# Optimization experiments

Hardware: AMD Instinct MI355X
Metric: run time of the kernel (lower is better)

The kernel has to match this reference:

```python
import jax, jax.numpy as jnp
import numpy as np

N, E, F, H, C = 50000, 800000, 128, 128, 40


def gcn_conv(x, edge_index, W, b):
    """PyG-style GCNConv: add self-loops, symmetric normalization, scatter-add."""
    n = x.shape[0]
    loop = jnp.arange(n, dtype=edge_index.dtype)
    src = jnp.concatenate([edge_index[0], loop])  # [E+N] source nodes
    dst = jnp.concatenate([edge_index[1], loop])  # [E+N] target nodes
    deg = jax.ops.segment_sum(jnp.ones_like(src, dtype=x.dtype), dst, num_segments=n)
    dinv = jnp.where(deg > 0, jax.lax.rsqrt(jnp.maximum(deg, 1e-12)), 0.0)
    norm = dinv[src] * dinv[dst]                  # [E+N]
    h = x @ W                                     # [N, out]
    msg = h[src] * norm[:, None]                  # [E+N, out]
    return jax.ops.segment_sum(msg, dst, num_segments=n) + b


def setup_inputs() -> dict:
    key = jax.random.key(0)
    ks = jax.random.split(key, 8)
    x = jax.random.normal(ks[0], (N, F), dtype=jnp.float32)
    edge_index = jax.random.randint(ks[1], (2, E), 0, N, dtype=jnp.int32)
    s = lambda fan_in: 1.0 / np.sqrt(fan_in)
    W1 = jax.random.normal(ks[2], (F, H), dtype=jnp.float32) * s(F)
    b1 = jax.random.normal(ks[3], (H,), dtype=jnp.float32) * 0.01
    W2 = jax.random.normal(ks[4], (H, C), dtype=jnp.float32) * s(H)
    b2 = jax.random.normal(ks[5], (C,), dtype=jnp.float32) * 0.01
    Wlin = jax.random.normal(ks[6], (C, C), dtype=jnp.float32) * s(C)
    blin = jax.random.normal(ks[7], (C,), dtype=jnp.float32) * 0.01
    return {"x": x, "edge_index": edge_index, "W1": W1, "b1": b1,
            "W2": W2, "b2": b2, "Wlin": Wlin, "blin": blin}


def reference(x, edge_index, W1, b1, W2, b2, Wlin, blin):
    h1 = jax.nn.relu(gcn_conv(x, edge_index, W1, b1))
    h2 = jax.nn.relu(gcn_conv(h1, edge_index, W2, b2))
    out = h2 @ Wlin + blin
    return (h2, out)
```

## Files before the change

### kernel.cpp

```cpp
#include <hip/hip_runtime.h>


constexpr int FDIM = 128;
constexpr int CDIM = 40;
constexpr int NPB  = 64;
constexpr int MAXNB = 1024;
constexpr int CH   = 4096;

typedef _Float16 h8  __attribute__((ext_vector_type(8)));
typedef _Float16 h4  __attribute__((ext_vector_type(4)));
typedef float    f4  __attribute__((ext_vector_type(4)));

static inline size_t AL512(size_t x) { return (x + 511) & ~size_t(511); }

__global__ __launch_bounds__(256) void k_bhist(const int* __restrict__ dst,
        int* __restrict__ bcnt, int E, int nb) {
    __shared__ int h[MAXNB];
    for (int i = threadIdx.x; i < nb; i += 256) h[i] = 0;
    __syncthreads();
    for (int i = blockIdx.x * 256 + threadIdx.x; i < E; i += gridDim.x * 256)
        atomicAdd(&h[dst[i] >> 6], 1);
    __syncthreads();
    for (int i = threadIdx.x; i < nb; i += 256) {
        int c = h[i];
        if (c) atomicAdd(&bcnt[i], c);
    }
}

__global__ __launch_bounds__(1024) void k_bscan(const int* __restrict__ bcnt,
        int* __restrict__ bbase, int* __restrict__ bcur, int nb, int E) {
    __shared__ int tmp[1024];
    int t = threadIdx.x;
    int v = (t < nb) ? bcnt[t] : 0;
    tmp[t] = v;
    __syncthreads();
    for (int o = 1; o < 1024; o <<= 1) {
        int u = (t >= o) ? tmp[t - o] : 0;
        __syncthreads();
        tmp[t] += u;
        __syncthreads();
    }
    if (t < nb) { int b = tmp[t] - v; bbase[t] = b; bcur[t] = b; }
    if (t == 0) bbase[nb] = E;
}

__global__ __launch_bounds__(256) void k_partition(const int* __restrict__ src,
        const int* __restrict__ dst, int* __restrict__ bcur,
        unsigned* __restrict__ eb, int E, int nb) {
    __shared__ int hcnt[MAXNB];
    __shared__ int gb[MAXNB];
    int e0 = blockIdx.x * CH;
    int cnt = min(CH, E - e0);
    for (int i = threadIdx.x; i < nb; i += 256) hcnt[i] = 0;
    __syncthreads();
    for (int i = threadIdx.x; i < cnt; i += 256)
        atomicAdd(&hcnt[dst[e0 + i] >> 6], 1);
    __syncthreads();
    for (int i = threadIdx.x; i < nb; i += 256) {
        int c = hcnt[i];
        if (c) gb[i] = atomicAdd(&bcur[i], c);
        hcnt[i] = 0;
    }
    __syncthreads();
    for (int i = threadIdx.x; i < cnt; i += 256) {
        int d = dst[e0 + i], b = d >> 6;
        int p = atomicAdd(&hcnt[b], 1);
        eb[gb[b] + p] = ((unsigned)src[e0 + i] << 6) | (unsigned)(d & 63);
    }
}

__global__ __launch_bounds__(256) void k_bucket_csr(const unsigned* __restrict__ eb,
        const int* __restrict__ bbase, int* __restrict__ offs,
        float* __restrict__ dinv, int* __restrict__ ss, int n) {
    __shared__ int cnt[NPB];
    __shared__ int cur[NPB];
    int b = blockIdx.x;
    int beg = bbase[b], end = bbase[b + 1];
    if (threadIdx.x < NPB) cnt[threadIdx.x] = 0;
    __syncthreads();
    for (int i = beg + threadIdx.x; i < end; i += 256)
        atomicAdd(&cnt[eb[i] & 63], 1);
    __syncthreads();
    if (threadIdx.x < NPB) {
        int v = cnt[threadIdx.x];
        int s = v;
#pragma unroll
        for (int o = 1; o < NPB; o <<= 1) {
            int u = __shfl_up(s, o, 64);
            if (threadIdx.x >= (unsigned)o) s += u;
        }
        int e0 = beg + s - v;
        cur[threadIdx.x] = e0;
        int node = b * NPB + threadIdx.x;
        if (node < n) {
            offs[node] = e0;
            dinv[node] = rsqrtf((float)v + 1.0f);
        }
    }
    __syncthreads();
    for (int i = beg + threadIdx.x; i < end; i += 256) {
        unsigned p = eb[i];
        int pos = atomicAdd(&cur[p & 63], 1);
        ss[pos] = (int)(p >> 6);
    }
}

__global__ __launch_bounds__(256) void k_prep(const float* __restrict__ W1,
        const float* __restrict__ W2, _Float16* __restrict__ W1t,
        _Float16* __restrict__ W2t) {
    int i = blockIdx.x * 256 + threadIdx.x;
    if (i < 128 * 128) {
        int c = i >> 7, k = i & 127;
        W1t[c * 128 + k] = (_Float16)W1[k * 128 + c];
    }
    int j = i - 128 * 128;
    if (j >= 0 && j < 64 * 128) {
        int c = j >> 7, k = j & 127;
        W2t[c * 128 + k] = (c < CDIM) ? (_Float16)W2[k * CDIM + c] : (_Float16)0.f;
    }
}

__global__ __launch_bounds__(256) void k_gemm1(const float* __restrict__ X,
        const _Float16* __restrict__ W1t, const float* __restrict__ dinv,
        _Float16* __restrict__ Hp, int n) {
    __shared__ _Float16 xh[64][136];
    __shared__ _Float16 wt[128][136];
    int t = threadIdx.x;
    int r0 = blockIdx.x * 64;
    for (int i = t; i < 64 * 32; i += 256) {
        int r = i >> 5, c4 = (i & 31) * 4;
        int gr = r0 + r;
        float4 v = make_float4(0.f, 0.f, 0.f, 0.f);
        if (gr < n) v = *(const float4*)&X[(size_t)gr * 128 + c4];
        h4 hv; hv[0] = (_Float16)v.x; hv[1] = (_Float16)v.y;
               hv[2] = (_Float16)v.z; hv[3] = (_Float16)v.w;
        *(h4*)&xh[r][c4] = hv;
    }
    for (int i = t; i < 128 * 16; i += 256) {
        int r = i >> 4, c8 = (i & 15) * 8;
        *(uint4*)&wt[r][c8] = *(const uint4*)&W1t[r * 128 + c8];
    }
    __syncthreads();
    int wid = t >> 6, lane = t & 63;
    int fr = lane & 15, fg = lane >> 4;
    f4 acc[8];
#pragma unroll
    for (int ct = 0; ct < 8; ++ct) acc[ct] = (f4){0.f, 0.f, 0.f, 0.f};
#pragma unroll
    for (int ks = 0; ks < 4; ++ks) {
        h8 a = *(const h8*)&xh[wid * 16 + fr][ks * 32 + fg * 8];
#pragma unroll
        for (int ct = 0; ct < 8; ++ct) {
            h8 b = *(const h8*)&wt[ct * 16 + fr][ks * 32 + fg * 8];
            acc[ct] = __builtin_amdgcn_mfma_f32_16x16x32_f16(a, b, acc[ct], 0, 0, 0);
        }
    }
    int rbase = r0 + wid * 16 + fg * 4;
    float dv[4];
#pragma unroll
    for (int rg = 0; rg < 4; ++rg) dv[rg] = (rbase + rg < n) ? dinv[rbase + rg] : 0.f;
#pragma unroll
    for (int ct = 0; ct < 8; ++ct)
#pragma unroll
        for (int rg = 0; rg < 4; ++rg) {
            int gr = rbase + rg;
            if (gr < n) Hp[(size_t)gr * 128 + ct * 16 + fr] = (_Float16)(acc[ct][rg] * dv[rg]);
        }
}

__global__ __launch_bounds__(256) void k_agg128(const int* __restrict__ ss,
        const int* __restrict__ offs, const _Float16* __restrict__ hp,
        const float* __restrict__ b1, const float* __restrict__ dinv,
        _Float16* __restrict__ h1, int n, int E) {
    int w = (blockIdx.x * 256 + threadIdx.x) >> 6;
    int lane = threadIdx.x & 63;
    if (w >= n) return;
    int beg = offs[w];
    int end = (w == n - 1) ? E : offs[w + 1];
    const h8* hpv = (const h8*)hp;
    int g = lane >> 4, c = lane & 15;
    h8 sv = hpv[(size_t)w * 16 + c];
    float acc[8];
#pragma unroll
    for (int i = 0; i < 8; ++i) acc[i] = (g == 0) ? (float)sv[i] : 0.f;
    int j = beg;
    for (; j + 7 < end; j += 8) {
        int s0 = ss[j + g];
        int s1 = ss[j + 4 + g];
        h8 v0 = hpv[(size_t)s0 * 16 + c];
        h8 v1 = hpv[(size_t)s1 * 16 + c];
#pragma unroll
        for (int i = 0; i < 8; ++i) acc[i] += (float)v0[i] + (float)v1[i];
    }
    for (; j < end; j += 4) {
        int idx = j + g;
        if (idx < end) {
            int s = ss[idx];
            h8 v = hpv[(size_t)s * 16 + c];
#pragma unroll
            for (int i = 0; i < 8; ++i) acc[i] += (float)v[i];
        }
    }
#pragma unroll
    for (int i = 0; i < 8; ++i) {
        acc[i] += __shfl_xor(acc[i], 16);
        acc[i] += __shfl_xor(acc[i], 32);
    }
    if (lane < 16) {
        float dvv = dinv[w];
        const float4 bb0 = *(const float4*)&b1[8 * lane];
        const float4 bb1 = *(const float4*)&b1[8 * lane + 4];
        h8 o;
        o[0] = (_Float16)fmaxf(fmaf(dvv, acc[0], bb0.x), 0.f);
        o[1] = (_Float16)fmaxf(fmaf(dvv, acc[1], bb0.y), 0.f);
        o[2] = (_Float16)fmaxf(fmaf(dvv, acc[2], bb0.z), 0.f);
        o[3] = (_Float16)fmaxf(fmaf(dvv, acc[3], bb0.w), 0.f);
        o[4] = (_Float16)fmaxf(fmaf(dvv, acc[4], bb1.x), 0.f);
        o[5] = (_Float16)fmaxf(fmaf(dvv, acc[5], bb1.y), 0.f);
        o[6] = (_Float16)fmaxf(fmaf(dvv, acc[6], bb1.z), 0.f);
        o[7] = (_Float16)fmaxf(fmaf(dvv, acc[7], bb1.w), 0.f);
        *(h8*)&h1[(size_t)w * 128 + 8 * lane] = o;
    }
}

__global__ __launch_bounds__(256) void k_gemm2(const _Float16* __restrict__ H1,
        const _Float16* __restrict__ W2t, const float* __restrict__ dinv,
        _Float16* __restrict__ Hp2, int n) {
    __shared__ _Float16 xh[64][136];
    __shared__ _Float16 wt[64][136];
    int t = threadIdx.x;
    int r0 = blockIdx.x * 64;
    for (int i = t; i < 64 * 16; i += 256) {
        int r = i >> 4, c8 = (i & 15) * 8;
        int gr = r0 + r;
        uint4 v = make_uint4(0u, 0u, 0u, 0u);
        if (gr < n) v = *(const uint4*)&H1[(size_t)gr * 128 + c8];
        *(uint4*)&xh[r][c8] = v;
    }
    for (int i = t; i < 64 * 16; i += 256) {
        int r = i >> 4, c8 = (i & 15) * 8;
        *(uint4*)&wt[r][c8] = *(const uint4*)&W2t[r * 128 + c8];
    }
    __syncthreads();
    int wid = t >> 6, lane = t & 63;
    int fr = lane & 15, fg = lane >> 4;
    f4 acc[4];
#pragma unroll
    for (int ct = 0; ct < 4; ++ct) acc[ct] = (f4){0.f, 0.f, 0.f, 0.f};
#pragma unroll
    for (int ks = 0; ks < 4; ++ks) {
        h8 a = *(const h8*)&xh[wid * 16 + fr][ks * 32 + fg * 8];
#pragma unroll
        for (int ct = 0; ct < 4; ++ct) {
            h8 b = *(const h8*)&wt[ct * 16 + fr][ks * 32 + fg * 8];
            acc[ct] = __builtin_amdgcn_mfma_f32_16x16x32_f16(a, b, acc[ct], 0, 0, 0);
        }
    }
    int rbase = r0 + wid * 16 + fg * 4;
    float dv[4];
#pragma unroll
    for (int rg = 0; rg < 4; ++rg) dv[rg] = (rbase + rg < n) ? dinv[rbase + rg] : 0.f;
#pragma unroll
    for (int ct = 0; ct < 4; ++ct)
#pragma unroll
        for (int rg = 0; rg < 4; ++rg) {
            int gr = rbase + rg;
            if (gr < n) Hp2[(size_t)gr * 64 + ct * 16 + fr] = (_Float16)(acc[ct][rg] * dv[rg]);
        }
}

__global__ __launch_bounds__(256) void k_agg40(const int* __restrict__ ss,
        const int* __restrict__ offs, const _Float16* __restrict__ hp,
        const float* __restrict__ b2, const float* __restrict__ dinv,
        float* __restrict__ h2out, int n, int E) {
    int w = (blockIdx.x * 256 + threadIdx.x) >> 6;
    int lane = threadIdx.x & 63;
    if (w >= n) return;
    int beg = offs[w];
    int end = (w == n - 1) ? E : offs[w + 1];
    const h8* hpv = (const h8*)hp;
    int g = lane >> 3, c = lane & 7;
    h8 sv = hpv[(size_t)w * 8 + c];
    float acc[8];
#pragma unroll
    for (int i = 0; i < 8; ++i) acc[i] = (g == 0) ? (float)sv[i] : 0.f;
    int j = beg;
    for (; j + 15 < end; j += 16) {
        int s0 = ss[j + g];
        int s1 = ss[j + 8 + g];
        h8 v0 = hpv[(size_t)s0 * 8 + c];
        h8 v1 = hpv[(size_t)s1 * 8 + c];
#pragma unroll
        for (int i = 0; i < 8; ++i) acc[i] += (float)v0[i] + (float)v1[i];
    }
    for (; j < end; j += 8) {
        int idx = j + g;
        if (idx < end) {
            int s = ss[idx];
            h8 v = hpv[(size_t)s * 8 + c];
#pragma unroll
            for (int i = 0; i < 8; ++i) acc[i] += (float)v[i];
        }
    }
#pragma unroll
    for (int i = 0; i < 8; ++i) {
        acc[i] += __shfl_xor(acc[i], 8);
        acc[i] += __shfl_xor(acc[i], 16);
        acc[i] += __shfl_xor(acc[i], 32);
    }
    if (lane < 5) {
        float dvv = dinv[w];
        const float4 bb0 = *(const float4*)&b2[8 * lane];
        const float4 bb1 = *(const float4*)&b2[8 * lane + 4];
        float4 r0, r1;
        r0.x = fmaxf(fmaf(dvv, acc[0], bb0.x), 0.f);
        r0.y = fmaxf(fmaf(dvv, acc[1], bb0.y), 0.f);
        r0.z = fmaxf(fmaf(dvv, acc[2], bb0.z), 0.f);
        r0.w = fmaxf(fmaf(dvv, acc[3], bb0.w), 0.f);
        r1.x = fmaxf(fmaf(dvv, acc[4], bb1.x), 0.f);
        r1.y = fmaxf(fmaf(dvv, acc[5], bb1.y), 0.f);
        r1.z = fmaxf(fmaf(dvv, acc[6], bb1.z), 0.f);
        r1.w = fmaxf(fmaf(dvv, acc[7], bb1.w), 0.f);
        *(float4*)&h2out[(size_t)w * CDIM + 8 * lane] = r0;
        *(float4*)&h2out[(size_t)w * CDIM + 8 * lane + 4] = r1;
    }
}

__global__ __launch_bounds__(256) void k_final(const float* __restrict__ h2,
        const float* __restrict__ Wlin, const float* __restrict__ blin,
        float* __restrict__ lin_out, int n) {
    __shared__ float wl[CDIM * CDIM];
    __shared__ float hs[32 * CDIM];
    int t = threadIdx.x;
    int r0 = blockIdx.x * 32;
    for (int i = t; i < CDIM * CDIM; i += 256) wl[i] = Wlin[i];
    int lim = n * CDIM - r0 * CDIM;
    for (int i = t; i < 32 * CDIM; i += 256)
        hs[i] = (i < lim) ? h2[(size_t)r0 * CDIM + i] : 0.f;
    __syncthreads();
    for (int i = t; i < 32 * CDIM; i += 256) {
        int r = i / CDIM, c = i % CDIM;
        int gr = r0 + r;
        if (gr >= n) continue;
        float acc = blin[c];
#pragma unroll
        for (int k = 0; k < CDIM; ++k) acc = fmaf(hs[r * CDIM + k], wl[k * CDIM + c], acc);
        lin_out[(size_t)gr * CDIM + c] = acc;
    }
}

extern "C" void kernel_launch(void* const* d_in, const int* in_sizes, int n_in,
                              void* d_out, int out_size, void* d_ws, size_t ws_size,
                              hipStream_t stream) {
    const float* x    = (const float*)d_in[0];
    const int*   ei   = (const int*)d_in[1];
    const float* W1   = (const float*)d_in[2];
    const float* b1   = (const float*)d_in[3];
    const float* W2   = (const float*)d_in[4];
    const float* b2   = (const float*)d_in[5];
    const float* Wlin = (const float*)d_in[6];
    const float* blin = (const float*)d_in[7];
    float* out = (float*)d_out;

    const int n = in_sizes[0] / FDIM;
    const int E = in_sizes[1] / 2;
    const int* src = ei;
    const int* dst = ei + E;
    const int nb = (n + NPB - 1) / NPB;

    char* ws = (char*)d_ws;
    size_t off = 0;
    int*       bcnt  = (int*)(ws + off);       off = AL512(off + (size_t)nb * 4);
    int*       bbase = (int*)(ws + off);       off = AL512(off + (size_t)(nb + 1) * 4);
    int*       bcur  = (int*)(ws + off);       off = AL512(off + (size_t)nb * 4);
    unsigned*  eb    = (unsigned*)(ws + off);  off = AL512(off + (size_t)E * 4);
    int*       offs  = (int*)(ws + off);       off = AL512(off + (size_t)n * 4);
    int*       ss    = (int*)(ws + off);       off = AL512(off + (size_t)E * 4);
    float*     dinv  = (float*)(ws + off);     off = AL512(off + (size_t)n * 4);
    _Float16*  W1t   = (_Float16*)(ws + off);  off = AL512(off + (size_t)128 * 128 * 2);
    _Float16*  W2t   = (_Float16*)(ws + off);  off = AL512(off + (size_t)64 * 128 * 2);
    _Float16*  hp1   = (_Float16*)(ws + off);  off = AL512(off + (size_t)n * FDIM * 2);
    _Float16*  h1h   = (_Float16*)(ws + off);  off = AL512(off + (size_t)n * FDIM * 2);
    _Float16*  hp2   = (_Float16*)(ws + off);  off = AL512(off + (size_t)n * 64 * 2);
    (void)ws_size; (void)n_in; (void)out_size;

    float* h2_out  = out;
    float* lin_out = out + (size_t)n * CDIM;

    k_prep<<<(128 * 128 + 64 * 128 + 255) / 256, 256, 0, stream>>>(W1, W2, W1t, W2t);
    hipMemsetAsync(bcnt, 0, (size_t)nb * 4, stream);
    k_bhist<<<256, 256, 0, stream>>>(dst, bcnt, E, nb);
    k_bscan<<<1, 1024, 0, stream>>>(bcnt, bbase, bcur, nb, E);
    k_partition<<<(E + CH - 1) / CH, 256, 0, stream>>>(src, dst, bcur, eb, E, nb);
    k_bucket_csr<<<nb, 256, 0, stream>>>(eb, bbase, offs, dinv, ss, n);

    k_gemm1<<<(n + 63) / 64, 256, 0, stream>>>(x, W1t, dinv, hp1, n);
    k_agg128<<<(n * 64 + 255) / 256, 256, 0, stream>>>(ss, offs, hp1, b1, dinv, h1h, n, E);

    k_gemm2<<<(n + 63) / 64, 256, 0, stream>>>(h1h, W2t, dinv, hp2, n);
    k_agg40<<<(n * 64 + 255) / 256, 256, 0, stream>>>(ss, offs, hp2, b2, dinv, h2_out, n, E);

    k_final<<<(n + 31) / 32, 256, 0, stream>>>(h2_out, Wlin, blin, lin_out, n);
}
```

Before: 150.5 us.

## Fuse final linear layer into agg40, fold memset into prep, deepen gather unroll

The final 40x40 linear layer is computed inside the second aggregation kernel. Each wavefront broadcasts its h2 row through shuffles and each lane produces one output column, which removes the k_final launch and the re-read of h2. The bucket-count memset is folded into k_prep to drop one stream operation. Both aggregation kernels gain a 4-way unrolled gather loop so more independent loads are in flight. The cost is extra global Wlin reads per wavefront (cache-resident) and higher register use.

```diff
diff --git a/kernel.cpp b/kernel.cpp
--- a/kernel.cpp
+++ b/kernel.cpp
@@ -12,6 +12,22 @@
 typedef float    f4  __attribute__((ext_vector_type(4)));
 
 static inline size_t AL512(size_t x) { return (x + 511) & ~size_t(511); }
+
+__global__ __launch_bounds__(256) void k_prep(const float* __restrict__ W1,
+        const float* __restrict__ W2, _Float16* __restrict__ W1t,
+        _Float16* __restrict__ W2t, int* __restrict__ bcnt, int nb) {
+    int i = blockIdx.x * 256 + threadIdx.x;
+    if (i < nb) bcnt[i] = 0;
+    if (i < 128 * 128) {
+        int c = i >> 7, k = i & 127;
+        W1t[c * 128 + k] = (_Float16)W1[k * 128 + c];
+    }
+    int j = i - 128 * 128;
+    if (j >= 0 && j < 64 * 128) {
+        int c = j >> 7, k = j & 127;
+        W2t[c * 128 + k] = (c < CDIM) ? (_Float16)W2[k * CDIM + c] : (_Float16)0.f;
+    }
+}
 
 __global__ __launch_bounds__(256) void k_bhist(const int* __restrict__ dst,
         int* __restrict__ bcnt, int E, int nb) {
@@ -102,21 +118,6 @@
         unsigned p = eb[i];
         int pos = atomicAdd(&cur[p & 63], 1);
         ss[pos] = (int)(p >> 6);
-    }
-}
-
-__global__ __launch_bounds__(256) void k_prep(const float* __restrict__ W1,
-        const float* __restrict__ W2, _Float16* __restrict__ W1t,
-        _Float16* __restrict__ W2t) {
-    int i = blockIdx.x * 256 + threadIdx.x;
-    if (i < 128 * 128) {
-        int c = i >> 7, k = i & 127;
-        W1t[c * 128 + k] = (_Float16)W1[k * 128 + c];
-    }
-    int j = i - 128 * 128;
-    if (j >= 0 && j < 64 * 128) {
-        int c = j >> 7, k = j & 127;
-        W2t[c * 128 + k] = (c < CDIM) ? (_Float16)W2[k * CDIM + c] : (_Float16)0.f;
     }
 }
 
@@ -184,6 +185,19 @@
 #pragma unroll
     for (int i = 0; i < 8; ++i) acc[i] = (g == 0) ? (float)sv[i] : 0.f;
     int j = beg;
+    for (; j + 15 < end; j += 16) {
+        int s0 = ss[j + g];
+        int s1 = ss[j + 4 + g];
+        int s2 = ss[j + 8 + g];
+        int s3 = ss[j + 12 + g];
+        h8 v0 = hpv[(size_t)s0 * 16 + c];
+        h8 v1 = hpv[(size_t)s1 * 16 + c];
+        h8 v2 = hpv[(size_t)s2 * 16 + c];
+        h8 v3 = hpv[(size_t)s3 * 16 + c];
+#pragma unroll
+        for (int i = 0; i < 8; ++i)
+            acc[i] += ((float)v0[i] + (float)v1[i]) + ((float)v2[i] + (float)v3[i]);
+    }
     for (; j + 7 < end; j += 8) {
         int s0 = ss[j + g];
         int s1 = ss[j + 4 + g];
@@ -272,7 +286,8 @@
 __global__ __launch_bounds__(256) void k_agg40(const int* __restrict__ ss,
         const int* __restrict__ offs, const _Float16* __restrict__ hp,
         const float* __restrict__ b2, const float* __restrict__ dinv,
-        float* __restrict__ h2out, int n, int E) {
+        const float* __restrict__ Wlin, const float* __restrict__ blin,
+        float* __restrict__ h2out, float* __restrict__ lin_out, int n, int E) {
     int w = (blockIdx.x * 256 + threadIdx.x) >> 6;
     int lane = threadIdx.x & 63;
     if (w >= n) return;
@@ -285,6 +300,19 @@
 #pragma unroll
     for (int i = 0; i < 8; ++i) acc[i] = (g == 0) ? (float)sv[i] : 0.f;
     int j = beg;
+    for (; j + 31 < end; j += 32) {
+        int s0 = ss[j + g];
+        int s1 = ss[j + 8 + g];
+        int s2 = ss[j + 16 + g];
+        int s3 = ss[j + 24 + g];
+        h8 v0 = hpv[(size_t)s0 * 8 + c];
+        h8 v1 = hpv[(size_t)s1 * 8 + c];
+        h8 v2 = hpv[(size_t)s2 * 8 + c];
+        h8 v3 = hpv[(size_t)s3 * 8 + c];
+#pragma unroll
+        for (int i = 0; i < 8; ++i)
+            acc[i] += ((float)v0[i] + (float)v1[i]) + ((float)v2[i] + (float)v3[i]);
+    }
     for (; j + 15 < end; j += 16) {
         int s0 = ss[j + g];
         int s1 = ss[j + 8 + g];
@@ -308,45 +336,39 @@
         acc[i] += __shfl_xor(acc[i], 16);
         acc[i] += __shfl_xor(acc[i], 32);
     }
+    float dvv = dinv[w];
+    float hv[8];
+    if (c < 5) {
+        const float4 bb0 = *(const float4*)&b2[8 * c];
+        const float4 bb1 = *(const float4*)&b2[8 * c + 4];
+        hv[0] = fmaxf(fmaf(dvv, acc[0], bb0.x), 0.f);
+        hv[1] = fmaxf(fmaf(dvv, acc[1], bb0.y), 0.f);
+        hv[2] = fmaxf(fmaf(dvv, acc[2], bb0.z), 0.f);
+        hv[3] = fmaxf(fmaf(dvv, acc[3], bb0.w), 0.f);
+        hv[4] = fmaxf(fmaf(dvv, acc[4], bb1.x), 0.f);
+        hv[5] = fmaxf(fmaf(dvv, acc[5], bb1.y), 0.f);
+        hv[6] = fmaxf(fmaf(dvv, acc[6], bb1.z), 0.f);
+        hv[7] = fmaxf(fmaf(dvv, acc[7], bb1.w), 0.f);
+    } else {
+#pragma unroll
+        for (int i = 0; i < 8; ++i) hv[i] = 0.f;
+    }
     if (lane < 5) {
-        float dvv = dinv[w];
-        const float4 bb0 = *(const float4*)&b2[8 * lane];
-        const float4 bb1 = *(const float4*)&b2[8 * lane + 4];
-        float4 r0, r1;
-        r0.x = fmaxf(fmaf(dvv, acc[0], bb0.x), 0.f);
-        r0.y = fmaxf(fmaf(dvv, acc[1], bb0.y), 0.f);
-        r0.z = fmaxf(fmaf(dvv, acc[2], bb0.z), 0.f);
-        r0.w = fmaxf(fmaf(dvv, acc[3], bb0.w), 0.f);
-        r1.x = fmaxf(fmaf(dvv, acc[4], bb1.x), 0.f);
-        r1.y = fmaxf(fmaf(dvv, acc[5], bb1.y), 0.f);
-        r1.z = fmaxf(fmaf(dvv, acc[6], bb1.z), 0.f);
-        r1.w = fmaxf(fmaf(dvv, acc[7], bb1.w), 0.f);
-        *(float4*)&h2out[(size_t)w * CDIM + 8 * lane] = r0;
-        *(float4*)&h2out[(size_t)w * CDIM + 8 * lane + 4] = r1;
-    }
-}
-
-__global__ __launch_bounds__(256) void k_final(const float* __restrict__ h2,
-        const float* __restrict__ Wlin, const float* __restrict__ blin,
-        float* __restrict__ lin_out, int n) {
-    __shared__ float wl[CDIM * CDIM];
-    __shared__ float hs[32 * CDIM];
-    int t = threadIdx.x;
-    int r0 = blockIdx.x * 32;
-    for (int i = t; i < CDIM * CDIM; i += 256) wl[i] = Wlin[i];
-    int lim = n * CDIM - r0 * CDIM;
-    for (int i = t; i < 32 * CDIM; i += 256)
-        hs[i] = (i < lim) ? h2[(size_t)r0 * CDIM + i] : 0.f;
-    __syncthreads();
-    for (int i = t; i < 32 * CDIM; i += 256) {
-        int r = i / CDIM, c = i % CDIM;
-        int gr = r0 + r;
-        if (gr >= n) continue;
-        float acc = blin[c];
-#pragma unroll
-        for (int k = 0; k < CDIM; ++k) acc = fmaf(hs[r * CDIM + k], wl[k * CDIM + c], acc);
-        lin_out[(size_t)gr * CDIM + c] = acc;
-    }
+        *(float4*)&h2out[(size_t)w * CDIM + 8 * lane] =
+            make_float4(hv[0], hv[1], hv[2], hv[3]);
+        *(float4*)&h2out[(size_t)w * CDIM + 8 * lane + 4] =
+            make_float4(hv[4], hv[5], hv[6], hv[7]);
+    }
+    float o = (lane < CDIM) ? blin[lane] : 0.f;
+#pragma unroll
+    for (int kc = 0; kc < 5; ++kc) {
+#pragma unroll
+        for (int i = 0; i < 8; ++i) {
+            float hk = __shfl(hv[i], kc);
+            if (lane < CDIM) o = fmaf(hk, Wlin[(8 * kc + i) * CDIM + lane], o);
+        }
+    }
+    if (lane < CDIM) lin_out[(size_t)w * CDIM + lane] = o;
 }
 
 extern "C" void kernel_launch(void* const* d_in, const int* in_sizes, int n_in,
@@ -387,8 +409,7 @@
     float* h2_out  = out;
     float* lin_out = out + (size_t)n * CDIM;
 
-    k_prep<<<(128 * 128 + 64 * 128 + 255) / 256, 256, 0, stream>>>(W1, W2, W1t, W2t);
-    hipMemsetAsync(bcnt, 0, (size_t)nb * 4, stream);
+    k_prep<<<(128 * 128 + 64 * 128 + 255) / 256, 256, 0, stream>>>(W1, W2, W1t, W2t, bcnt, nb);
     k_bhist<<<256, 256, 0, stream>>>(dst, bcnt, E, nb);
     k_bscan<<<1, 1024, 0, stream>>>(bcnt, bbase, bcur, nb, E);
     k_partition<<<(E + CH - 1) / CH, 256, 0, stream>>>(src, dst, bcur, eb, E, nb);
@@ -398,7 +419,6 @@
     k_agg128<<<(n * 64 + 255) / 256, 256, 0, stream>>>(ss, offs, hp1, b1, dinv, h1h, n, E);
 
     k_gemm2<<<(n + 63) / 64, 256, 0, stream>>>(h1h, W2t, dinv, hp2, n);
-    k_agg40<<<(n * 64 + 255) / 256, 256, 0, stream>>>(ss, offs, hp2, b2, dinv, h2_out, n, E);
-
-    k_final<<<(n + 31) / 32, 256, 0, stream>>>(h2_out, Wlin, blin, lin_out, n);
-}
+    k_agg40<<<(n * 64 + 255) / 256, 256, 0, stream>>>(ss, offs, hp2, b2, dinv,
+                                                      Wlin, blin, h2_out, lin_out, n, E);
+}
```

Result: slower. 172.1 us (+14.4%).

## Split gathered features into 32-column slabs and narrow neighbor indices to 16-bit

Applied to the files above, without the earlier changes.

Intermediate feature matrices are stored as separate 32-column planes, and aggregation blocks are ordered by plane so that each gather pass works on a smaller table that is more likely to stay cache-resident. Layer 2 is split into a 32-column plane and an 8-column plane, which drops the zero padding to 64 columns. Neighbor indices are stored as 16-bit values, halving index traffic, and the bucket-count memset is folded into the prep kernel. The cost is re-reading the CSR indices once per plane, and the 16-bit indices only work while the node count stays below 65536.

```diff
diff --git a/kernel.cpp b/kernel.cpp
--- a/kernel.cpp
+++ b/kernel.cpp
@@ -10,8 +10,25 @@
 typedef _Float16 h8  __attribute__((ext_vector_type(8)));
 typedef _Float16 h4  __attribute__((ext_vector_type(4)));
 typedef float    f4  __attribute__((ext_vector_type(4)));
+typedef unsigned short u16;
 
 static inline size_t AL512(size_t x) { return (x + 511) & ~size_t(511); }
+
+__global__ __launch_bounds__(256) void k_prep(const float* __restrict__ W1,
+        const float* __restrict__ W2, _Float16* __restrict__ W1t,
+        _Float16* __restrict__ W2t, int* __restrict__ bcnt, int nb) {
+    int i = blockIdx.x * 256 + threadIdx.x;
+    if (i < nb) bcnt[i] = 0;
+    if (i < 128 * 128) {
+        int c = i >> 7, k = i & 127;
+        W1t[c * 128 + k] = (_Float16)W1[k * 128 + c];
+    }
+    int j = i - 128 * 128;
+    if (j >= 0 && j < 48 * 128) {
+        int c = j >> 7, k = j & 127;
+        W2t[c * 128 + k] = (c < CDIM) ? (_Float16)W2[k * CDIM + c] : (_Float16)0.f;
+    }
+}
 
 __global__ __launch_bounds__(256) void k_bhist(const int* __restrict__ dst,
         int* __restrict__ bcnt, int E, int nb) {
@@ -71,7 +88,7 @@
 
 __global__ __launch_bounds__(256) void k_bucket_csr(const unsigned* __restrict__ eb,
         const int* __restrict__ bbase, int* __restrict__ offs,
-        float* __restrict__ dinv, int* __restrict__ ss, int n) {
+        float* __restrict__ dinv, u16* __restrict__ ss, int n) {
     __shared__ int cnt[NPB];
     __shared__ int cur[NPB];
     int b = blockIdx.x;
@@ -101,22 +118,7 @@
     for (int i = beg + threadIdx.x; i < end; i += 256) {
         unsigned p = eb[i];
         int pos = atomicAdd(&cur[p & 63], 1);
-        ss[pos] = (int)(p >> 6);
-    }
-}
-
-__global__ __launch_bounds__(256) void k_prep(const float* __restrict__ W1,
-        const float* __restrict__ W2, _Float16* __restrict__ W1t,
-        _Float16* __restrict__ W2t) {
-    int i = blockIdx.x * 256 + threadIdx.x;
-    if (i < 128 * 128) {
-        int c = i >> 7, k = i & 127;
-        W1t[c * 128 + k] = (_Float16)W1[k * 128 + c];
-    }
-    int j = i - 128 * 128;
-    if (j >= 0 && j < 64 * 128) {
-        int c = j >> 7, k = j & 127;
-        W2t[c * 128 + k] = (c < CDIM) ? (_Float16)W2[k * CDIM + c] : (_Float16)0.f;
+        ss[pos] = (u16)(p >> 6);
     }
 }
 
@@ -127,6 +129,7 @@
     __shared__ _Float16 wt[128][136];
     int t = threadIdx.x;
     int r0 = blockIdx.x * 64;
+    size_t qs = (size_t)n * 32;
     for (int i = t; i < 64 * 32; i += 256) {
         int r = i >> 5, c4 = (i & 31) * 4;
         int gr = r0 + r;
@@ -160,56 +163,74 @@
 #pragma unroll
     for (int rg = 0; rg < 4; ++rg) dv[rg] = (rbase + rg < n) ? dinv[rbase + rg] : 0.f;
 #pragma unroll
-    for (int ct = 0; ct < 8; ++ct)
+    for (int ct = 0; ct < 8; ++ct) {
+        int q = ct >> 1, cq = (ct & 1) * 16 + fr;
 #pragma unroll
         for (int rg = 0; rg < 4; ++rg) {
             int gr = rbase + rg;
-            if (gr < n) Hp[(size_t)gr * 128 + ct * 16 + fr] = (_Float16)(acc[ct][rg] * dv[rg]);
-        }
-}
-
-__global__ __launch_bounds__(256) void k_agg128(const int* __restrict__ ss,
+            if (gr < n) Hp[q * qs + (size_t)gr * 32 + cq] = (_Float16)(acc[ct][rg] * dv[rg]);
+        }
+    }
+}
+
+__global__ __launch_bounds__(256) void k_agg128(const u16* __restrict__ ss,
         const int* __restrict__ offs, const _Float16* __restrict__ hp,
         const float* __restrict__ b1, const float* __restrict__ dinv,
-        _Float16* __restrict__ h1, int n, int E) {
-    int w = (blockIdx.x * 256 + threadIdx.x) >> 6;
+        _Float16* __restrict__ h1, int n, int E, int nbq) {
+    int b = blockIdx.x;
+    int q = b / nbq;
+    int w = (b - q * nbq) * 4 + (threadIdx.x >> 6);
+    if (w >= n) return;
     int lane = threadIdx.x & 63;
-    if (w >= n) return;
+    int g = lane >> 2, c = lane & 3;
+    size_t qs = (size_t)n * 32;
+    const h8* base = (const h8*)(hp + q * qs);
     int beg = offs[w];
     int end = (w == n - 1) ? E : offs[w + 1];
-    const h8* hpv = (const h8*)hp;
-    int g = lane >> 4, c = lane & 15;
-    h8 sv = hpv[(size_t)w * 16 + c];
     float acc[8];
-#pragma unroll
-    for (int i = 0; i < 8; ++i) acc[i] = (g == 0) ? (float)sv[i] : 0.f;
+    if (g == 0) {
+        h8 sv = base[(size_t)w * 4 + c];
+#pragma unroll
+        for (int i = 0; i < 8; ++i) acc[i] = (float)sv[i];
+    } else {
+#pragma unroll
+        for (int i = 0; i < 8; ++i) acc[i] = 0.f;
+    }
     int j = beg;
-    for (; j + 7 < end; j += 8) {
-        int s0 = ss[j + g];
-        int s1 = ss[j + 4 + g];
-        h8 v0 = hpv[(size_t)s0 * 16 + c];
-        h8 v1 = hpv[(size_t)s1 * 16 + c];
-#pragma unroll
-        for (int i = 0; i < 8; ++i) acc[i] += (float)v0[i] + (float)v1[i];
-    }
-    for (; j < end; j += 4) {
+    for (; j + 16 < end; j += 32) {
+        int i0 = j + g, i1 = j + 16 + g;
+        int s0 = ss[i0];
+        bool p1 = i1 < end;
+        int s1 = p1 ? (int)ss[i1] : s0;
+        h8 v0 = base[(size_t)s0 * 4 + c];
+        h8 v1 = base[(size_t)s1 * 4 + c];
+#pragma unroll
+        for (int i = 0; i < 8; ++i) {
+            acc[i] += (float)v0[i];
+            if (p1) acc[i] += (float)v1[i];
+        }
+    }
+    for (; j < end; j += 16) {
         int idx = j + g;
         if (idx < end) {
             int s = ss[idx];
-            h8 v = hpv[(size_t)s * 16 + c];
+            h8 v = base[(size_t)s * 4 + c];
 #pragma unroll
             for (int i = 0; i < 8; ++i) acc[i] += (float)v[i];
         }
     }
 #pragma unroll
     for (int i = 0; i < 8; ++i) {
+        acc[i] += __shfl_xor(acc[i], 4);
+        acc[i] += __shfl_xor(acc[i], 8);
         acc[i] += __shfl_xor(acc[i], 16);
         acc[i] += __shfl_xor(acc[i], 32);
     }
-    if (lane < 16) {
+    if (lane < 4) {
         float dvv = dinv[w];
-        const float4 bb0 = *(const float4*)&b1[8 * lane];
-        const float4 bb1 = *(const float4*)&b1[8 * lane + 4];
+        int col0 = q * 32 + lane * 8;
+        const float4 bb0 = *(const float4*)&b1[col0];
+        const float4 bb1 = *(const float4*)&b1[col0 + 4];
         h8 o;
         o[0] = (_Float16)fmaxf(fmaf(dvv, acc[0], bb0.x), 0.f);
         o[1] = (_Float16)fmaxf(fmaf(dvv, acc[1], bb0.y), 0.f);
@@ -219,39 +240,43 @@
         o[5] = (_Float16)fmaxf(fmaf(dvv, acc[5], bb1.y), 0.f);
         o[6] = (_Float16)fmaxf(fmaf(dvv, acc[6], bb1.z), 0.f);
         o[7] = (_Float16)fmaxf(fmaf(dvv, acc[7], bb1.w), 0.f);
-        *(h8*)&h1[(size_t)w * 128 + 8 * lane] = o;
+        ((h8*)(h1 + q * qs))[(size_t)w * 4 + lane] = o;
     }
 }
 
 __global__ __launch_bounds__(256) void k_gemm2(const _Float16* __restrict__ H1,
         const _Float16* __restrict__ W2t, const float* __restrict__ dinv,
-        _Float16* __restrict__ Hp2, int n) {
+        _Float16* __restrict__ Hp2a, _Float16* __restrict__ Hp2b, int n) {
     __shared__ _Float16 xh[64][136];
-    __shared__ _Float16 wt[64][136];
+    __shared__ _Float16 wt[48][136];
     int t = threadIdx.x;
     int r0 = blockIdx.x * 64;
+    size_t qs = (size_t)n * 32;
     for (int i = t; i < 64 * 16; i += 256) {
-        int r = i >> 4, c8 = (i & 15) * 8;
+        int r = i >> 4, c8 = i & 15;
         int gr = r0 + r;
         uint4 v = make_uint4(0u, 0u, 0u, 0u);
-        if (gr < n) v = *(const uint4*)&H1[(size_t)gr * 128 + c8];
-        *(uint4*)&xh[r][c8] = v;
-    }
-    for (int i = t; i < 64 * 16; i += 256) {
+        if (gr < n) {
+            int q = c8 >> 2, within = (c8 & 3) * 8;
+            v = *(const uint4*)&H1[q * qs + (size_t)gr * 32 + within];
+        }
+        *(uint4*)&xh[r][c8 * 8] = v;
+    }
+    for (int i = t; i < 48 * 16; i += 256) {
         int r = i >> 4, c8 = (i & 15) * 8;
         *(uint4*)&wt[r][c8] = *(const uint4*)&W2t[r * 128 + c8];
     }
     __syncthreads();
     int wid = t >> 6, lane = t & 63;
     int fr = lane & 15, fg = lane >> 4;
-    f4 acc[4];
-#pragma unroll
-    for (int ct = 0; ct < 4; ++ct) acc[ct] = (f4){0.f, 0.f, 0.f, 0.f};
+    f4 acc[3];
+#pragma unroll
+    for (int ct = 0; ct < 3; ++ct) acc[ct] = (f4){0.f, 0.f, 0.f, 0.f};
 #pragma unroll
     for (int ks = 0; ks < 4; ++ks) {
         h8 a = *(const h8*)&xh[wid * 16 + fr][ks * 32 + fg * 8];
 #pragma unroll
-        for (int ct = 0; ct < 4; ++ct) {
+        for (int ct = 0; ct < 3; ++ct) {
             h8 b = *(const h8*)&wt[ct * 16 + fr][ks * 32 + fg * 8];
             acc[ct] = __builtin_amdgcn_mfma_f32_16x16x32_f16(a, b, acc[ct], 0, 0, 0);
         }
@@ -261,68 +286,126 @@
 #pragma unroll
     for (int rg = 0; rg < 4; ++rg) dv[rg] = (rbase + rg < n) ? dinv[rbase + rg] : 0.f;
 #pragma unroll
-    for (int ct = 0; ct < 4; ++ct)
-#pragma unroll
-        for (int rg = 0; rg < 4; ++rg) {
-            int gr = rbase + rg;
-            if (gr < n) Hp2[(size_t)gr * 64 + ct * 16 + fr] = (_Float16)(acc[ct][rg] * dv[rg]);
-        }
-}
-
-__global__ __launch_bounds__(256) void k_agg40(const int* __restrict__ ss,
-        const int* __restrict__ offs, const _Float16* __restrict__ hp,
-        const float* __restrict__ b2, const float* __restrict__ dinv,
-        float* __restrict__ h2out, int n, int E) {
-    int w = (blockIdx.x * 256 + threadIdx.x) >> 6;
+    for (int rg = 0; rg < 4; ++rg) {
+        int gr = rbase + rg;
+        if (gr >= n) continue;
+        Hp2a[(size_t)gr * 32 + fr]      = (_Float16)(acc[0][rg] * dv[rg]);
+        Hp2a[(size_t)gr * 32 + 16 + fr] = (_Float16)(acc[1][rg] * dv[rg]);
+        if (fr < 8) Hp2b[(size_t)gr * 8 + fr] = (_Float16)(acc[2][rg] * dv[rg]);
+    }
+}
+
+__global__ __launch_bounds__(256) void k_agg40(const u16* __restrict__ ss,
+        const int* __restrict__ offs, const _Float16* __restrict__ hpa,
+        const _Float16* __restrict__ hpb, const float* __restrict__ b2,
+        const float* __restrict__ dinv, float* __restrict__ h2out,
+        int n, int E, int nbq) {
+    int b = blockIdx.x;
+    int q = b / nbq;
+    int w = (b - q * nbq) * 4 + (threadIdx.x >> 6);
+    if (w >= n) return;
     int lane = threadIdx.x & 63;
-    if (w >= n) return;
     int beg = offs[w];
     int end = (w == n - 1) ? E : offs[w + 1];
-    const h8* hpv = (const h8*)hp;
-    int g = lane >> 3, c = lane & 7;
-    h8 sv = hpv[(size_t)w * 8 + c];
-    float acc[8];
-#pragma unroll
-    for (int i = 0; i < 8; ++i) acc[i] = (g == 0) ? (float)sv[i] : 0.f;
-    int j = beg;
-    for (; j + 15 < end; j += 16) {
-        int s0 = ss[j + g];
-        int s1 = ss[j + 8 + g];
-        h8 v0 = hpv[(size_t)s0 * 8 + c];
-        h8 v1 = hpv[(size_t)s1 * 8 + c];
-#pragma unroll
-        for (int i = 0; i < 8; ++i) acc[i] += (float)v0[i] + (float)v1[i];
-    }
-    for (; j < end; j += 8) {
-        int idx = j + g;
-        if (idx < end) {
-            int s = ss[idx];
-            h8 v = hpv[(size_t)s * 8 + c];
-#pragma unroll
-            for (int i = 0; i < 8; ++i) acc[i] += (float)v[i];
-        }
-    }
-#pragma unroll
-    for (int i = 0; i < 8; ++i) {
-        acc[i] += __shfl_xor(acc[i], 8);
-        acc[i] += __shfl_xor(acc[i], 16);
-        acc[i] += __shfl_xor(acc[i], 32);
-    }
-    if (lane < 5) {
-        float dvv = dinv[w];
-        const float4 bb0 = *(const float4*)&b2[8 * lane];
-        const float4 bb1 = *(const float4*)&b2[8 * lane + 4];
-        float4 r0, r1;
-        r0.x = fmaxf(fmaf(dvv, acc[0], bb0.x), 0.f);
-        r0.y = fmaxf(fmaf(dvv, acc[1], bb0.y), 0.f);
-        r0.z = fmaxf(fmaf(dvv, acc[2], bb0.z), 0.f);
-        r0.w = fmaxf(fmaf(dvv, acc[3], bb0.w), 0.f);
-        r1.x = fmaxf(fmaf(dvv, acc[4], bb1.x), 0.f);
-        r1.y = fmaxf(fmaf(dvv, acc[5], bb1.y), 0.f);
-        r1.z = fmaxf(fmaf(dvv, acc[6], bb1.z), 0.f);
-        r1.w = fmaxf(fmaf(dvv, acc[7], bb1.w), 0.f);
-        *(float4*)&h2out[(size_t)w * CDIM + 8 * lane] = r0;
-        *(float4*)&h2out[(size_t)w * CDIM + 8 * lane + 4] = r1;
+    if (q == 0) {
+        int g = lane >> 2, c = lane & 3;
+        const h8* base = (const h8*)hpa;
+        float acc[8];
+        if (g == 0) {
+            h8 sv = base[(size_t)w * 4 + c];
+#pragma unroll
+            for (int i = 0; i < 8; ++i) acc[i] = (float)sv[i];
+        } else {
+#pragma unroll
+            for (int i = 0; i < 8; ++i) acc[i] = 0.f;
+        }
+        int j = beg;
+        for (; j + 16 < end; j += 32) {
+            int i0 = j + g, i1 = j + 16 + g;
+            int s0 = ss[i0];
+            bool p1 = i1 < end;
+            int s1 = p1 ? (int)ss[i1] : s0;
+            h8 v0 = base[(size_t)s0 * 4 + c];
+            h8 v1 = base[(size_t)s1 * 4 + c];
+#pragma unroll
+            for (int i = 0; i < 8; ++i) {
+                acc[i] += (float)v0[i];
+                if (p1) acc[i] += (float)v1[i];
+            }
+        }
+        for (; j < end; j += 16) {
+            int idx = j + g;
+            if (idx < end) {
+                int s = ss[idx];
+                h8 v = base[(size_t)s * 4 + c];
+#pragma unroll
+                for (int i = 0; i < 8; ++i) acc[i] += (float)v[i];
+            }
+        }
+#pragma unroll
+        for (int i = 0; i < 8; ++i) {
+            acc[i] += __shfl_xor(acc[i], 4);
+            acc[i] += __shfl_xor(acc[i], 8);
+            acc[i] += __shfl_xor(acc[i], 16);
+            acc[i] += __shfl_xor(acc[i], 32);
+        }
+        if (lane < 4) {
+            float dvv = dinv[w];
+            int col0 = lane * 8;
+            const float4 bb0 = *(const float4*)&b2[col0];
+            const float4 bb1 = *(const float4*)&b2[col0 + 4];
+            float4 r0, r1;
+            r0.x = fmaxf(fmaf(dvv, acc[0], bb0.x), 0.f);
+            r0.y = fmaxf(fmaf(dvv, acc[1], bb0.y), 0.f);
+            r0.z = fmaxf(fmaf(dvv, acc[2], bb0.z), 0.f);
+            r0.w = fmaxf(fmaf(dvv, acc[3], bb0.w), 0.f);
+            r1.x = fmaxf(fmaf(dvv, acc[4], bb1.x), 0.f);
+            r1.y = fmaxf(fmaf(dvv, acc[5], bb1.y), 0.f);
+            r1.z = fmaxf(fmaf(dvv, acc[6], bb1.z), 0.f);
+            r1.w = fmaxf(fmaf(dvv, acc[7], bb1.w), 0.f);
+            *(float4*)&h2out[(size_t)w * CDIM + col0] = r0;
+            *(float4*)&h2out[(size_t)w * CDIM + col0 + 4] = r1;
+        }
+    } else {
+        const h8* base = (const h8*)hpb;
+        h8 selfv = base[w];
+        float acc[8];
+#pragma unroll
+        for (int i = 0; i < 8; ++i) acc[i] = 0.f;
+        for (int j = beg; j < end; j += 64) {
+            int idx = j + lane;
+            if (idx < end) {
+                int s = ss[idx];
+                h8 v = base[s];
+#pragma unroll
+                for (int i = 0; i < 8; ++i) acc[i] += (float)v[i];
+            }
+        }
+#pragma unroll
+        for (int i = 0; i < 8; ++i) {
+            acc[i] += __shfl_xor(acc[i], 1);
+            acc[i] += __shfl_xor(acc[i], 2);
+            acc[i] += __shfl_xor(acc[i], 4);
+            acc[i] += __shfl_xor(acc[i], 8);
+            acc[i] += __shfl_xor(acc[i], 16);
+            acc[i] += __shfl_xor(acc[i], 32);
+        }
+        if (lane == 0) {
+            float dvv = dinv[w];
+            const float4 bb0 = *(const float4*)&b2[32];
+            const float4 bb1 = *(const float4*)&b2[36];
+            float4 r0, r1;
+            r0.x = fmaxf(fmaf(dvv, acc[0] + (float)selfv[0], bb0.x), 0.f);
+            r0.y = fmaxf(fmaf(dvv, acc[1] + (float)selfv[1], bb0.y), 0.f);
+            r0.z = fmaxf(fmaf(dvv, acc[2] + (float)selfv[2], bb0.z), 0.f);
+            r0.w = fmaxf(fmaf(dvv, acc[3] + (float)selfv[3], bb0.w), 0.f);
+            r1.x = fmaxf(fmaf(dvv, acc[4] + (float)selfv[4], bb1.x), 0.f);
+            r1.y = fmaxf(fmaf(dvv, acc[5] + (float)selfv[5], bb1.y), 0.f);
+            r1.z = fmaxf(fmaf(dvv, acc[6] + (float)selfv[6], bb1.z), 0.f);
+            r1.w = fmaxf(fmaf(dvv, acc[7] + (float)selfv[7], bb1.w), 0.f);
+            *(float4*)&h2out[(size_t)w * CDIM + 32] = r0;
+            *(float4*)&h2out[(size_t)w * CDIM + 36] = r1;
+        }
     }
 }
 
@@ -367,6 +450,7 @@
     const int* src = ei;
     const int* dst = ei + E;
     const int nb = (n + NPB - 1) / NPB;
+    const int nbq = (n + 3) / 4;
 
     char* ws = (char*)d_ws;
     size_t off = 0;
@@ -375,30 +459,30 @@
     int*       bcur  = (int*)(ws + off);       off = AL512(off + (size_t)nb * 4);
     unsigned*  eb    = (unsigned*)(ws + off);  off = AL512(off + (size_t)E * 4);
     int*       offs  = (int*)(ws + off);       off = AL512(off + (size_t)n * 4);
-    int*       ss    = (int*)(ws + off);       off = AL512(off + (size_t)E * 4);
+    u16*       ss    = (u16*)(ws + off);       off = AL512(off + (size_t)E * 2);
     float*     dinv  = (float*)(ws + off);     off = AL512(off + (size_t)n * 4);
     _Float16*  W1t   = (_Float16*)(ws + off);  off = AL512(off + (size_t)128 * 128 * 2);
-    _Float16*  W2t   = (_Float16*)(ws + off);  off = AL512(off + (size_t)64 * 128 * 2);
-    _Float16*  hp1   = (_Float16*)(ws + off);  off = AL512(off + (size_t)n * FDIM * 2);
-    _Float16*  h1h   = (_Float16*)(ws + off);  off = AL512(off + (size_t)n * FDIM * 2);
-    _Float16*  hp2   = (_Float16*)(ws + off);  off = AL512(off + (size_t)n * 64 * 2);
+    _Float16*  W2t   = (_Float16*)(ws + off);  off = AL512(off + (size_t)48 * 128 * 2);
+    _Float16*  hp1   = (_Float16*)(ws + off);  off = AL512(off + (size_t)n * 128 * 2);
+    _Float16*  h1h   = (_Float16*)(ws + off);  off = AL512(off + (size_t)n * 128 * 2);
+    _Float16*  hp2a  = (_Float16*)(ws + off);  off = AL512(off + (size_t)n * 32 * 2);
+    _Float16*  hp2b  = (_Float16*)(ws + off);  off = AL512(off + (size_t)n * 8 * 2);
     (void)ws_size; (void)n_in; (void)out_size;
 
     float* h2_out  = out;
     float* lin_out = out + (size_t)n * CDIM;
 
-    k_prep<<<(128 * 128 + 64 * 128 + 255) / 256, 256, 0, stream>>>(W1, W2, W1t, W2t);
-    hipMemsetAsync(bcnt, 0, (size_t)nb * 4, stream);
+    k_prep<<<(128 * 128 + 48 * 128 + 255) / 256, 256, 0, stream>>>(W1, W2, W1t, W2t, bcnt, nb);
     k_bhist<<<256, 256, 0, stream>>>(dst, bcnt, E, nb);
     k_bscan<<<1, 1024, 0, stream>>>(bcnt, bbase, bcur, nb, E);
     k_partition<<<(E + CH - 1) / CH, 256, 0, stream>>>(src, dst, bcur, eb, E, nb);
     k_bucket_csr<<<nb, 256, 0, stream>>>(eb, bbase, offs, dinv, ss, n);
 
     k_gemm1<<<(n + 63) / 64, 256, 0, stream>>>(x, W1t, dinv, hp1, n);
-    k_agg128<<<(n * 64 + 255) / 256, 256, 0, stream>>>(ss, offs, hp1, b1, dinv, h1h, n, E);
-
-    k_gemm2<<<(n + 63) / 64, 256, 0, stream>>>(h1h, W2t, dinv, hp2, n);
-    k_agg40<<<(n * 64 + 255) / 256, 256, 0, stream>>>(ss, offs, hp2, b2, dinv, h2_out, n, E);
+    k_agg128<<<4 * nbq, 256, 0, stream>>>(ss, offs, hp1, b1, dinv, h1h, n, E, nbq);
+
+    k_gemm2<<<(n + 63) / 64, 256, 0, stream>>>(h1h, W2t, dinv, hp2a, hp2b, n);
+    k_agg40<<<2 * nbq, 256, 0, stream>>>(ss, offs, hp2a, hp2b, b2, dinv, h2_out, n, E, nbq);
 
     k_final<<<(n + 31) / 32, 256, 0, stream>>>(h2_out, Wlin, blin, lin_out, n);
 }
```

Result: slower. 204.3 us (+35.7%).
